# Optimization experiments

Hardware: AMD Instinct MI355X
Metric: run time of the kernel (lower is better)

## Reference

```python
import jax, jax.numpy as jnp
import numpy as np
import math

B, NQ, NKV, D, H, KP = 4, 8192, 8192, 256, 8, 256
HD = D // H


def setup_inputs() -> dict:
    key = jax.random.key(0)
    ks = jax.random.split(key, 8)
    s = 1.0 / math.sqrt(D)
    return {
        "x1": jax.random.normal(ks[0], (B, NQ, D), dtype=jnp.float32),
        "x2": jax.random.normal(ks[1], (NKV, D), dtype=jnp.float32),
        "Wq": jax.random.normal(ks[2], (D, D), dtype=jnp.float32) * s,
        "Wk": jax.random.normal(ks[3], (D, D), dtype=jnp.float32) * s,
        "Wv": jax.random.normal(ks[4], (D, D), dtype=jnp.float32) * s,
        "Wo": jax.random.normal(ks[5], (D, D), dtype=jnp.float32) * s,
        "E": jax.random.normal(ks[6], (NKV, KP), dtype=jnp.float32) * (1.0 / math.sqrt(NKV)),
        "F": jax.random.normal(ks[7], (NKV, KP), dtype=jnp.float32) * (1.0 / math.sqrt(NKV)),
    }


def reference(x1, x2, Wq, Wk, Wv, Wo, E, F):
    # x1: [B, NQ, D] queries; x2: [NKV, D] shared cross-attention context
    q = x1 @ Wq                               # [B, NQ, D]
    k = x2 @ Wk                               # [NKV, D]
    v = x2 @ Wv                               # [NKV, D]
    # Linformer low-rank compression along the KV sequence axis
    k_low = jnp.einsum('nd,nk->kd', k, E)     # [KP, D]
    v_low = jnp.einsum('nd,nk->kd', v, F)     # [KP, D]
    qh = q.reshape(B, NQ, H, HD)
    kh = k_low.reshape(KP, H, HD)
    vh = v_low.reshape(KP, H, HD)
    scale = 1.0 / math.sqrt(HD)
    scores = jnp.einsum('bqhd,khd->bhqk', qh, kh) * scale  # [B, H, NQ, KP]
    attn = jax.nn.softmax(scores, axis=-1)
    out = jnp.einsum('bhqk,khd->bqhd', attn, vh)           # [B, NQ, H, HD]
    out = out.reshape(B, NQ, D)
    return out @ Wo
```

## Files before the change

### kernel.cpp

```cpp
#include <hip/hip_runtime.h>
#include <math.h>
#include <stdint.h>


typedef unsigned short ushort_t;
typedef __attribute__((ext_vector_type(8))) short bf16x8;
typedef __attribute__((ext_vector_type(8))) _Float16 f16x8;
typedef __attribute__((ext_vector_type(4))) float f32x4;

__device__ __forceinline__ f32x4 MFMA(bf16x8 a, bf16x8 b, f32x4 c) {
  return __builtin_amdgcn_mfma_f32_16x16x32_bf16(a, b, c, 0, 0, 0);
}
__device__ __forceinline__ f32x4 MFMA_H(f16x8 a, f16x8 b, f32x4 c) {
  return __builtin_amdgcn_mfma_f32_16x16x32_f16(a, b, c, 0, 0, 0);
}
__device__ __forceinline__ ushort_t f2bf(float x) {
  uint32_t u = __float_as_uint(x);
  u += 0x7fffu + ((u >> 16) & 1u);
  return (ushort_t)(u >> 16);
}
#define GLDS(gsrc, ldst)                                                    \
  __builtin_amdgcn_global_load_lds(                                         \
      (const __attribute__((address_space(1))) uint32_t*)(const void*)(gsrc), \
      (__attribute__((address_space(3))) uint32_t*)(void*)(ldst), 16, 0, 0)

#define STAGE_ROW(u) \
  (((((u) >> 2) ^ ((u) >> 4)) & 1) | (((u) >> 2) & 6) | (((u) >> 5) << 3))
#define STAGE_G(u) \
  ((((u) ^ ((u) >> 2) ^ ((u) >> 4)) & 1) | (((((u) >> 1) ^ ((u) >> 3)) & 1) << 1))

__global__ __launch_bounds__(256) void k_prep_all(
    const float* __restrict__ x2, const float* __restrict__ E,
    const float* __restrict__ F, const float* __restrict__ Wq,
    const float* __restrict__ Wk, const float* __restrict__ Wv,
    const float* __restrict__ Wo, _Float16* __restrict__ xt,
    ushort_t* __restrict__ wqt, ushort_t* __restrict__ wot,
    _Float16* __restrict__ wkt, _Float16* __restrict__ wvt) {
  __shared__ float tile[64][65];
  const int t = threadIdx.x;
  const int z = blockIdx.z;
  if (z < 3) {
    const int n0 = blockIdx.x * 64;
    const int c0 = blockIdx.y * 64;
    const float* __restrict__ src = (z == 0) ? x2 : (z == 1) ? E : F;
    _Float16* __restrict__ dst = xt + (size_t)z * 2097152;
    const int rr = t >> 4, cc = (t & 15) * 4;
#pragma unroll
    for (int i = 0; i < 4; ++i) {
      float4 v = *(const float4*)&src[(size_t)(n0 + rr + 16 * i) * 256 + c0 + cc];
      tile[cc + 0][rr + 16 * i] = v.x;
      tile[cc + 1][rr + 16 * i] = v.y;
      tile[cc + 2][rr + 16 * i] = v.z;
      tile[cc + 3][rr + 16 * i] = v.w;
    }
    __syncthreads();
#pragma unroll
    for (int rnd = 0; rnd < 2; ++rnd) {
      const int u = rnd * 256 + t;
      const int c = u >> 3, r0 = (u & 7) * 8;
      f16x8 h;
#pragma unroll
      for (int j = 0; j < 8; ++j) h[j] = (_Float16)tile[c][r0 + j];
      *(f16x8*)&dst[(size_t)(c0 + c) * 8192 + n0 + r0] = h;
    }
  } else {
    if (blockIdx.x >= 16) return;
    const int m = blockIdx.y;
    const float* __restrict__ src = (m == 0) ? Wq : (m == 1) ? Wo
                                  : (m == 2) ? Wk : Wv;
    const int tr = (blockIdx.x >> 2) * 64;
    const int tc = (blockIdx.x & 3) * 64;
    const int rr = t >> 4, cc = (t & 15) * 4;
#pragma unroll
    for (int i = 0; i < 4; ++i) {
      float4 v = *(const float4*)&src[(size_t)(tr + rr + 16 * i) * 256 + tc + cc];
      tile[cc + 0][rr + 16 * i] = v.x;
      tile[cc + 1][rr + 16 * i] = v.y;
      tile[cc + 2][rr + 16 * i] = v.z;
      tile[cc + 3][rr + 16 * i] = v.w;
    }
    __syncthreads();
#pragma unroll
    for (int rnd = 0; rnd < 2; ++rnd) {
      const int u = rnd * 256 + t;
      const int nl = u >> 3, kl = (u & 7) * 8;
      if (m < 2) {
        const float sc = (m == 0) ? 0.25503488f : 1.0f;
        bf16x8 hv;
#pragma unroll
        for (int j = 0; j < 8; ++j) hv[j] = (short)f2bf(tile[nl][kl + j] * sc);
        ushort_t* dst = (m == 0) ? wqt : wot;
        *(bf16x8*)&dst[(size_t)(tc + nl) * 256 + tr + kl] = hv;
      } else {
        f16x8 hv;
#pragma unroll
        for (int j = 0; j < 8; ++j) hv[j] = (_Float16)tile[nl][kl + j];
        _Float16* dst = (m == 2) ? wkt : wvt;
        *(f16x8*)&dst[(size_t)(tc + nl) * 256 + tr + kl] = hv;
      }
    }
  }
}

__global__ __launch_bounds__(512, 2) void k_mega1(
    const float* __restrict__ x1, const _Float16* __restrict__ xt,
    const ushort_t* __restrict__ wqt, ushort_t* __restrict__ Qf,
    float* __restrict__ part) {
  __shared__ __align__(16) char smem[65536];
  const int t = threadIdx.x;
  const int wv = t >> 6, ln = t & 63;
  const int l15 = ln & 15, g = ln >> 4;

  if (blockIdx.x < 64) {
    const int bid2 = blockIdx.x;
    const int which = bid2 & 1;
    const int chunk = (bid2 >> 1) & 15;
    const int kp0 = (bid2 >> 5) * 128;
    const int n0 = chunk * 512;
    const _Float16* __restrict__ A = xt + (size_t)(1 + which) * 2097152;
    const _Float16* __restrict__ B = xt;
    const int wr = wv >> 2, wc = wv & 3;

    auto stage = [&](int buf, int st) {
#pragma unroll
      for (int r3 = 0; r3 < 3; ++r3) {
        const int u = r3 * 512 + t;
        if (u < 512) {
          const int row = u >> 2, j = u & 3;
          GLDS(A + (size_t)(kp0 + row) * 8192 + n0 + st * 32 +
                   ((j ^ (row & 3)) << 3),
               smem + buf * 24576 + u * 16);
        } else {
          const int uu = u - 512;
          const int row = uu >> 2, j = uu & 3;
          GLDS(B + (size_t)row * 8192 + n0 + st * 32 + ((j ^ (row & 3)) << 3),
               smem + buf * 24576 + 8192 + uu * 16);
        }
      }
    };

    f32x4 acc[4][4];
#pragma unroll
    for (int i = 0; i < 4; ++i)
#pragma unroll
      for (int j = 0; j < 4; ++j) acc[i][j] = {0.f, 0.f, 0.f, 0.f};

    stage(0, 0);
    __syncthreads();
    for (int st = 0; st < 16; ++st) {
      if (st < 15) stage((st + 1) & 1, st + 1);
      const char* la = smem + (st & 1) * 24576;
      const char* lb = la + 8192;
      f16x8 af[4], bf[4];
#pragma unroll
      for (int i = 0; i < 4; ++i) {
        const int ra = wr * 64 + i * 16 + l15;
        af[i] = *(const f16x8*)(la + ra * 64 + ((g ^ (ra & 3)) << 4));
      }
#pragma unroll
      for (int j = 0; j < 4; ++j) {
        const int rb = wc * 64 + j * 16 + l15;
        bf[j] = *(const f16x8*)(lb + rb * 64 + ((g ^ (rb & 3)) << 4));
      }
#pragma unroll
      for (int i = 0; i < 4; ++i)
#pragma unroll
        for (int j = 0; j < 4; ++j) acc[i][j] = MFMA_H(af[i], bf[j], acc[i][j]);
      __syncthreads();
    }
    float* __restrict__ p = part + ((size_t)which * 16 + chunk) * 65536;
#pragma unroll
    for (int i = 0; i < 4; ++i)
#pragma unroll
      for (int j = 0; j < 4; ++j)
#pragma unroll
        for (int r = 0; r < 4; ++r)
          p[(size_t)(kp0 + wr * 64 + i * 16 + g * 4 + r) * 256 + wc * 64 +
            j * 16 + l15] = acc[i][j][r];
  } else {
    const int qb = blockIdx.x - 64;
    const size_t r0 = (size_t)qb * 128;
    auto stageq = [&](int buf, int ks) {
#pragma unroll
      for (int rnd = 0; rnd < 2; ++rnd) {
        const int u = rnd * 512 + t;
        const int n = u >> 2, j = u & 3;
        GLDS(wqt + n * 256 + ks * 32 + ((j ^ (n & 3)) << 3),
             smem + buf * 16384 + u * 16);
      }
    };
    f32x4 qacc[16];
#pragma unroll
    for (int i = 0; i < 16; ++i) qacc[i] = {0.f, 0.f, 0.f, 0.f};
    stageq(0, 0);
    const float* xrow = x1 + (r0 + wv * 16 + l15) * 256;
    float4 a0 = *(const float4*)(xrow + g * 8);
    float4 a1 = *(const float4*)(xrow + g * 8 + 4);
    __syncthreads();

    for (int ks = 0; ks < 8; ++ks) {
      if (ks < 7) stageq((ks + 1) & 1, ks + 1);
      bf16x8 afrag;
      afrag[0] = (short)f2bf(a0.x); afrag[1] = (short)f2bf(a0.y);
      afrag[2] = (short)f2bf(a0.z); afrag[3] = (short)f2bf(a0.w);
      afrag[4] = (short)f2bf(a1.x); afrag[5] = (short)f2bf(a1.y);
      afrag[6] = (short)f2bf(a1.z); afrag[7] = (short)f2bf(a1.w);
      if (ks < 7) {
        a0 = *(const float4*)(xrow + (ks + 1) * 32 + g * 8);
        a1 = *(const float4*)(xrow + (ks + 1) * 32 + g * 8 + 4);
      }
      const char* cw = smem + (ks & 1) * 16384;
#pragma unroll
      for (int tt = 0; tt < 16; ++tt) {
        bf16x8 bfr = *(const bf16x8*)(cw + (tt * 16 + l15) * 64 +
                                      ((g ^ (l15 & 3)) << 4));
        qacc[tt] = MFMA(afrag, bfr, qacc[tt]);
      }
      __syncthreads();
    }
    char* myq = smem + wv * 8192;
#pragma unroll
    for (int tt = 0; tt < 16; ++tt)
#pragma unroll
      for (int r = 0; r < 4; ++r) {
        const int gr = g * 4 + r;
        *(ushort_t*)(myq + gr * 512 +
                     (((tt * 16 + l15) * 2) ^ ((gr & 7) << 4))) =
            f2bf(qacc[tt][r]);
      }
    __builtin_amdgcn_sched_barrier(0);
    const int rt = qb * 8 + wv;
#pragma unroll
    for (int hh = 0; hh < 8; ++hh) {
      bf16x8 qf = *(const bf16x8*)(myq + l15 * 512 +
                                   ((hh * 64 + g * 16) ^ ((l15 & 7) << 4)));
      *(bf16x8*)&Qf[((size_t)(rt * 8 + hh) * 64 + ln) * 8] = qf;
    }
  }
}

__global__ __launch_bounds__(256) void k_reduce_part(
    const float* __restrict__ part, _Float16* __restrict__ ghh) {
  const int oid = blockIdx.x * 256 + threadIdx.x;
  const int which = oid >> 16;
  const int base = oid & 65535;
  const float* __restrict__ p = part + (size_t)which * 16 * 65536 + base;
  float s = 0.f;
#pragma unroll
  for (int c = 0; c < 16; ++c) s += p[c * 65536];
  ghh[oid] = (_Float16)s;
}

__global__ __launch_bounds__(256, 4) void k_lowproj2(
    const _Float16* __restrict__ ghh, const _Float16* __restrict__ wkt,
    const _Float16* __restrict__ wvt, ushort_t* __restrict__ klowA,
    ushort_t* __restrict__ vtb) {
  __shared__ __align__(16) _Float16 wstage[2][4096];
  const int t = threadIdx.x;
  const int wv = t >> 6, ln = t & 63;
  const int l15 = ln & 15, g = ln >> 4;
  const int which = blockIdx.y;
  const int r0 = blockIdx.x * 64;
  const _Float16* __restrict__ A = ghh + (size_t)which * 65536;
  const _Float16* __restrict__ W = which ? wvt : wkt;

  auto stage = [&](int row0, int colu, int buf) {
#pragma unroll
    for (int rnd = 0; rnd < 2; ++rnd) {
      const int u = rnd * 256 + wv * 64 + ln;
      const int row = STAGE_ROW(u);
      const int gg = STAGE_G(u);
      GLDS(W + (size_t)(row0 + row) * 256 + colu + gg * 8,
           &wstage[buf][(rnd * 256 + wv * 64) * 8]);
    }
  };

  f32x4 yacc[16];
#pragma unroll
  for (int i = 0; i < 16; ++i) yacc[i] = {0.f, 0.f, 0.f, 0.f};
  stage(0, 0, 0);
  const _Float16* arow = A + (size_t)(r0 + wv * 16 + l15) * 256;
  __syncthreads();
  for (int ci = 0; ci < 16; ++ci) {
    const int nh = ci & 1, ks = ci >> 1;
    if (ci < 15) stage(((ci + 1) & 1) * 128, ((ci + 1) >> 1) * 32, (ci + 1) & 1);
    f16x8 afrag = *(const f16x8*)(arow + ks * 32 + g * 8);
    const _Float16* cw = wstage[ci & 1];
#pragma unroll
    for (int tt = 0; tt < 8; ++tt) {
      f16x8 bfr = *(const f16x8*)&cw[((tt * 16 + l15) * 32 + g * 8) ^
                                     ((l15 & 7) << 3)];
      yacc[nh * 8 + tt] = MFMA_H(afrag, bfr, yacc[nh * 8 + tt]);
    }
    __syncthreads();
  }
#pragma unroll
  for (int tt = 0; tt < 16; ++tt)
#pragma unroll
    for (int r = 0; r < 4; ++r) {
      const int rowi = r0 + wv * 16 + g * 4 + r;
      const int c = tt * 16 + l15;
      const int hh = c >> 5, d = c & 31;
      const ushort_t val = f2bf(yacc[tt][r]);
      if (which == 0) {
        klowA[(hh << 13) + ((((rowi & 255) << 5) | d) ^ ((rowi & 7) << 3))] = val;
      } else {
        const int kh = (rowi >> 7) & 1, kl = rowi & 127;
        vtb[(((hh * 2 + kh) * 32 + d) << 7) + (kl ^ ((d & 7) << 3))] = val;
      }
    }
}

__global__ __launch_bounds__(512, 4) void k_attn(
    const ushort_t* __restrict__ Qf, const ushort_t* __restrict__ klowA,
    const ushort_t* __restrict__ vtb, ushort_t* __restrict__ O) {
  __shared__ __align__(16) ushort_t kv[16384];
  __shared__ __align__(16) uint32_t p_buf[8][320];
  __shared__ __align__(16) ushort_t o_sl[8][640];
  const int t = threadIdx.x;
  const int wv = t >> 6, ln = t & 63;
  const int l15 = ln & 15, g = ln >> 4;
  const int h = blockIdx.y;
  const size_t r0 = (size_t)blockIdx.x * 512;

  {
    const ushort_t* ksrc = klowA + h * 8192;
    const ushort_t* vsrc = vtb + h * 8192;
#pragma unroll
    for (int rnd = 0; rnd < 2; ++rnd) {
      const int ub = rnd * 512 + wv * 64;
      GLDS(ksrc + (ub + ln) * 8, &kv[ub * 8]);
    }
#pragma unroll
    for (int rnd = 0; rnd < 2; ++rnd) {
      const int ub = rnd * 512 + wv * 64;
      GLDS(vsrc + (ub + ln) * 8, &kv[8192 + ub * 8]);
    }
  }
  __syncthreads();

  for (int st = 0; st < 4; ++st) {
    const int rtb = blockIdx.x * 32 + st * 8 + wv;
    const bf16x8 qfrag = *(const bf16x8*)&Qf[((size_t)(rtb * 8 + h) * 64 + ln) * 8];
    f32x4 s[16];
#pragma unroll
    for (int tt = 0; tt < 16; ++tt) {
      bf16x8 kfr = *(const bf16x8*)&kv[((tt * 16 + l15) * 32 + g * 8) ^
                                       ((l15 & 7) << 3)];
      f32x4 z = {0.f, 0.f, 0.f, 0.f};
      s[tt] = MFMA(kfr, qfrag, z);
    }
    float sum = 0.f;
    uint32_t pw[16][2];
#pragma unroll
    for (int tt = 0; tt < 16; ++tt) {
      float e0 = exp2f(s[tt][0]), e1 = exp2f(s[tt][1]);
      float e2 = exp2f(s[tt][2]), e3 = exp2f(s[tt][3]);
      sum += (e0 + e1) + (e2 + e3);
      pw[tt][0] = (uint32_t)f2bf(e0) | ((uint32_t)f2bf(e1) << 16);
      pw[tt][1] = (uint32_t)f2bf(e2) | ((uint32_t)f2bf(e3) << 16);
    }
    sum += __shfl_xor(sum, 16);
    sum += __shfl_xor(sum, 32);
    const float rinv = 1.0f / sum;
    float rv[4];
#pragma unroll
    for (int r = 0; r < 4; ++r) rv[r] = __shfl(rinv, g * 4 + r);

    f32x4 oacc[2];
    oacc[0] = {0.f, 0.f, 0.f, 0.f};
    oacc[1] = {0.f, 0.f, 0.f, 0.f};
    uint32_t* pbw = &p_buf[wv][l15 * 20];
#pragma unroll
    for (int kh = 0; kh < 2; ++kh) {
      const char* cv = (const char*)&kv[8192 + kh * 4096];
#pragma unroll
      for (int ksl = 0; ksl < 4; ++ksl) {
        const int ks = kh * 4 + ksl;
        pbw[2 * g + 0] = pw[2 * ks][0];
        pbw[2 * g + 1] = pw[2 * ks][1];
        pbw[8 + 2 * g + 0] = pw[2 * ks + 1][0];
        pbw[8 + 2 * g + 1] = pw[2 * ks + 1][1];
        __builtin_amdgcn_sched_barrier(0);
        bf16x8 pfr = *(const bf16x8*)&p_buf[wv][l15 * 20 + 4 * g];
#pragma unroll
        for (int nt = 0; nt < 2; ++nt) {
          bf16x8 vfr = *(const bf16x8*)(cv + (nt * 16 + l15) * 256 +
                                        ((ksl * 64 + g * 16) ^ ((l15 & 7) << 4)));
          oacc[nt] = MFMA(pfr, vfr, oacc[nt]);
        }
        __builtin_amdgcn_sched_barrier(0);
      }
    }
#pragma unroll
    for (int nt = 0; nt < 2; ++nt)
#pragma unroll
      for (int r = 0; r < 4; ++r)
        o_sl[wv][(g * 4 + r) * 40 + nt * 16 + l15] = f2bf(oacc[nt][r] * rv[r]);
    __builtin_amdgcn_sched_barrier(0);
    {
      const int qr = ln >> 2, d0 = (ln & 3) * 8;
      bf16x8 ov = *(const bf16x8*)&o_sl[wv][qr * 40 + d0];
      *(bf16x8*)&O[(r0 + st * 128 + wv * 16 + qr) * 256 + h * 32 + d0] = ov;
    }
    __builtin_amdgcn_sched_barrier(0);
  }
}

__global__ __launch_bounds__(512, 2) void k_ogemm(
    const ushort_t* __restrict__ O, const ushort_t* __restrict__ wot,
    float* __restrict__ out) {
  __shared__ __align__(16) char smem[32768];
  const int t = threadIdx.x;
  const int wv = t >> 6, ln = t & 63;
  const int l15 = ln & 15, g = ln >> 4;
  const size_t r0 = (size_t)blockIdx.x * 128;

  auto stageo = [&](int buf, int ks) {
#pragma unroll
    for (int rnd = 0; rnd < 2; ++rnd) {
      const int u = rnd * 512 + t;
      const int n = u >> 2, j = u & 3;
      GLDS(wot + n * 256 + ks * 32 + ((j ^ (n & 3)) << 3),
           smem + buf * 16384 + u * 16);
    }
  };

  f32x4 yacc[16];
#pragma unroll
  for (int i = 0; i < 16; ++i) yacc[i] = {0.f, 0.f, 0.f, 0.f};
  stageo(0, 0);
  const ushort_t* arow = O + (r0 + wv * 16 + l15) * 256;
  bf16x8 afrag = *(const bf16x8*)(arow + g * 8);
  __syncthreads();

  for (int ks = 0; ks < 8; ++ks) {
    if (ks < 7) stageo((ks + 1) & 1, ks + 1);
    bf16x8 cA = afrag;
    if (ks < 7) afrag = *(const bf16x8*)(arow + (ks + 1) * 32 + g * 8);
    const char* cw = smem + (ks & 1) * 16384;
#pragma unroll
    for (int tt = 0; tt < 16; ++tt) {
      bf16x8 bfr = *(const bf16x8*)(cw + (tt * 16 + l15) * 64 +
                                    ((g ^ (l15 & 3)) << 4));
      yacc[tt] = MFMA(cA, bfr, yacc[tt]);
    }
    __syncthreads();
  }
#pragma unroll
  for (int tt = 0; tt < 16; ++tt)
#pragma unroll
    for (int r = 0; r < 4; ++r)
      out[(r0 + wv * 16 + g * 4 + r) * 256 + tt * 16 + l15] = yacc[tt][r];
}

extern "C" void kernel_launch(void* const* d_in, const int* in_sizes, int n_in,
                              void* d_out, int out_size, void* d_ws, size_t ws_size,
                              hipStream_t stream) {
  const float* x1 = (const float*)d_in[0];
  const float* x2 = (const float*)d_in[1];
  const float* Wq = (const float*)d_in[2];
  const float* Wk = (const float*)d_in[3];
  const float* Wv = (const float*)d_in[4];
  const float* Wo = (const float*)d_in[5];
  const float* E  = (const float*)d_in[6];
  const float* F  = (const float*)d_in[7];
  float* out = (float*)d_out;
  float* ws = (float*)d_ws;
  _Float16* ghh = (_Float16*)ws;
  ushort_t* wqt = (ushort_t*)(ws + 65536);
  ushort_t* wot = (ushort_t*)(ws + 98304);
  _Float16* wkt = (_Float16*)(ws + 131072);
  _Float16* wvt = (_Float16*)(ws + 163840);
  ushort_t* klowA = (ushort_t*)(ws + 196608);
  ushort_t* vtb = (ushort_t*)(ws + 229376);
  float* part = ws + 262144;
  ushort_t* Qf = (ushort_t*)(ws + 2359296);
  _Float16* xt = (_Float16*)(ws + 6553600);
  ushort_t* O = (ushort_t*)(ws + 6553600);

  k_prep_all<<<dim3(128, 4, 4), 256, 0, stream>>>(x2, E, F, Wq, Wk, Wv, Wo, xt,
                                                  wqt, wot, wkt, wvt);
  k_mega1<<<320, 512, 0, stream>>>(x1, xt, wqt, Qf, part);
  k_reduce_part<<<512, 256, 0, stream>>>(part, ghh);
  k_lowproj2<<<dim3(4, 2), 256, 0, stream>>>(ghh, wkt, wvt, klowA, vtb);
  k_attn<<<dim3(64, 8), 512, 0, stream>>>(Qf, klowA, vtb, O);
  k_ogemm<<<256, 512, 0, stream>>>(O, wot, out);
}
```

Before: 94.43 us.

## Fuse attention and output projection into one kernel with per-wave heads

Merges the attention kernel and the Wo output GEMM into a single kernel. Each block handles 64 rows with one wave per head, keeps the attention output in LDS instead of writing O to global memory, then runs the output projection from LDS. K/V fragments are now read straight from global memory instead of being staged in shared memory. This removes a launch and the round trip of the intermediate O buffer, but gives up LDS reuse of K/V and lowers occupancy.

```diff
diff --git a/kernel.cpp b/kernel.cpp
--- a/kernel.cpp
+++ b/kernel.cpp
@@ -311,44 +311,49 @@
     }
 }
 
-__global__ __launch_bounds__(512, 4) void k_attn(
+__global__ __launch_bounds__(512, 2) void k_attn_out(
     const ushort_t* __restrict__ Qf, const ushort_t* __restrict__ klowA,
-    const ushort_t* __restrict__ vtb, ushort_t* __restrict__ O) {
-  __shared__ __align__(16) ushort_t kv[16384];
+    const ushort_t* __restrict__ vtb, const ushort_t* __restrict__ wot,
+    float* __restrict__ out) {
+  __shared__ __align__(16) char o_lds[32768];
+  __shared__ __align__(16) char wstage[32768];
   __shared__ __align__(16) uint32_t p_buf[8][320];
-  __shared__ __align__(16) ushort_t o_sl[8][640];
   const int t = threadIdx.x;
   const int wv = t >> 6, ln = t & 63;
   const int l15 = ln & 15, g = ln >> 4;
-  const int h = blockIdx.y;
-  const size_t r0 = (size_t)blockIdx.x * 512;
-
-  {
-    const ushort_t* ksrc = klowA + h * 8192;
-    const ushort_t* vsrc = vtb + h * 8192;
+  const size_t r0 = (size_t)blockIdx.x * 64;
+  const int h = wv;
+
+  auto stageo = [&](int buf, int ks) {
 #pragma unroll
     for (int rnd = 0; rnd < 2; ++rnd) {
-      const int ub = rnd * 512 + wv * 64;
-      GLDS(ksrc + (ub + ln) * 8, &kv[ub * 8]);
-    }
-#pragma unroll
-    for (int rnd = 0; rnd < 2; ++rnd) {
-      const int ub = rnd * 512 + wv * 64;
-      GLDS(vsrc + (ub + ln) * 8, &kv[8192 + ub * 8]);
-    }
-  }
-  __syncthreads();
-
+      const int u = rnd * 512 + t;
+      const int n = u >> 2, j = u & 3;
+      GLDS(wot + n * 256 + ks * 32 + ((j ^ (n & 3)) << 3),
+           wstage + buf * 16384 + u * 16);
+    }
+  };
+
+  stageo(0, 0);
+
+  const ushort_t* kh_ = klowA + h * 8192;
+  const ushort_t* vh_ = vtb + h * 8192;
+  bf16x8 qfr[4];
+#pragma unroll
   for (int st = 0; st < 4; ++st) {
-    const int rtb = blockIdx.x * 32 + st * 8 + wv;
-    const bf16x8 qfrag = *(const bf16x8*)&Qf[((size_t)(rtb * 8 + h) * 64 + ln) * 8];
+    const int rt = blockIdx.x * 4 + st;
+    qfr[st] = *(const bf16x8*)&Qf[((size_t)(rt * 8 + h) * 64 + ln) * 8];
+  }
+
+#pragma unroll
+  for (int st = 0; st < 4; ++st) {
     f32x4 s[16];
 #pragma unroll
     for (int tt = 0; tt < 16; ++tt) {
-      bf16x8 kfr = *(const bf16x8*)&kv[((tt * 16 + l15) * 32 + g * 8) ^
-                                       ((l15 & 7) << 3)];
+      bf16x8 kfr = *(const bf16x8*)&kh_[(((tt * 16 + l15) * 32 + g * 8)) ^
+                                        ((l15 & 7) << 3)];
       f32x4 z = {0.f, 0.f, 0.f, 0.f};
-      s[tt] = MFMA(kfr, qfrag, z);
+      s[tt] = MFMA(kfr, qfr[st], z);
     }
     float sum = 0.f;
     uint32_t pw[16][2];
@@ -372,11 +377,11 @@
     oacc[1] = {0.f, 0.f, 0.f, 0.f};
     uint32_t* pbw = &p_buf[wv][l15 * 20];
 #pragma unroll
-    for (int kh = 0; kh < 2; ++kh) {
-      const char* cv = (const char*)&kv[8192 + kh * 4096];
+    for (int kh2 = 0; kh2 < 2; ++kh2) {
+      const char* cv = (const char*)(vh_ + kh2 * 4096);
 #pragma unroll
       for (int ksl = 0; ksl < 4; ++ksl) {
-        const int ks = kh * 4 + ksl;
+        const int ks = kh2 * 4 + ksl;
         pbw[2 * g + 0] = pw[2 * ks][0];
         pbw[2 * g + 1] = pw[2 * ks][1];
         pbw[8 + 2 * g + 0] = pw[2 * ks + 1][0];
@@ -395,63 +400,40 @@
 #pragma unroll
     for (int nt = 0; nt < 2; ++nt)
 #pragma unroll
-      for (int r = 0; r < 4; ++r)
-        o_sl[wv][(g * 4 + r) * 40 + nt * 16 + l15] = f2bf(oacc[nt][r] * rv[r]);
-    __builtin_amdgcn_sched_barrier(0);
-    {
-      const int qr = ln >> 2, d0 = (ln & 3) * 8;
-      bf16x8 ov = *(const bf16x8*)&o_sl[wv][qr * 40 + d0];
-      *(bf16x8*)&O[(r0 + st * 128 + wv * 16 + qr) * 256 + h * 32 + d0] = ov;
-    }
-    __builtin_amdgcn_sched_barrier(0);
-  }
-}
-
-__global__ __launch_bounds__(512, 2) void k_ogemm(
-    const ushort_t* __restrict__ O, const ushort_t* __restrict__ wot,
-    float* __restrict__ out) {
-  __shared__ __align__(16) char smem[32768];
-  const int t = threadIdx.x;
-  const int wv = t >> 6, ln = t & 63;
-  const int l15 = ln & 15, g = ln >> 4;
-  const size_t r0 = (size_t)blockIdx.x * 128;
-
-  auto stageo = [&](int buf, int ks) {
-#pragma unroll
-    for (int rnd = 0; rnd < 2; ++rnd) {
-      const int u = rnd * 512 + t;
-      const int n = u >> 2, j = u & 3;
-      GLDS(wot + n * 256 + ks * 32 + ((j ^ (n & 3)) << 3),
-           smem + buf * 16384 + u * 16);
-    }
-  };
-
-  f32x4 yacc[16];
-#pragma unroll
-  for (int i = 0; i < 16; ++i) yacc[i] = {0.f, 0.f, 0.f, 0.f};
-  stageo(0, 0);
-  const ushort_t* arow = O + (r0 + wv * 16 + l15) * 256;
-  bf16x8 afrag = *(const bf16x8*)(arow + g * 8);
+      for (int r = 0; r < 4; ++r) {
+        const int row = st * 16 + g * 4 + r;
+        const int cb = (h * 32 + nt * 16 + l15) * 2;
+        *(ushort_t*)(o_lds + row * 512 + (cb ^ ((row & 7) << 4))) =
+            f2bf(oacc[nt][r] * rv[r]);
+      }
+  }
   __syncthreads();
+
+  const int rg = wv >> 1, ch = wv & 1;
+  const int arow = rg * 16 + l15;
+  f32x4 yacc[8];
+#pragma unroll
+  for (int i = 0; i < 8; ++i) yacc[i] = {0.f, 0.f, 0.f, 0.f};
 
   for (int ks = 0; ks < 8; ++ks) {
     if (ks < 7) stageo((ks + 1) & 1, ks + 1);
-    bf16x8 cA = afrag;
-    if (ks < 7) afrag = *(const bf16x8*)(arow + (ks + 1) * 32 + g * 8);
-    const char* cw = smem + (ks & 1) * 16384;
-#pragma unroll
-    for (int tt = 0; tt < 16; ++tt) {
-      bf16x8 bfr = *(const bf16x8*)(cw + (tt * 16 + l15) * 64 +
-                                    ((g ^ (l15 & 3)) << 4));
-      yacc[tt] = MFMA(cA, bfr, yacc[tt]);
-    }
-    __syncthreads();
-  }
-#pragma unroll
-  for (int tt = 0; tt < 16; ++tt)
+    bf16x8 afrag = *(const bf16x8*)(o_lds + arow * 512 +
+                                    ((ks * 64 + g * 16) ^ ((arow & 7) << 4)));
+    const char* cw = wstage + (ks & 1) * 16384;
+#pragma unroll
+    for (int tt = 0; tt < 8; ++tt) {
+      const int n = ch * 128 + tt * 16 + l15;
+      bf16x8 bfr = *(const bf16x8*)(cw + n * 64 + ((g ^ (n & 3)) << 4));
+      yacc[tt] = MFMA(afrag, bfr, yacc[tt]);
+    }
+    __syncthreads();
+  }
+#pragma unroll
+  for (int tt = 0; tt < 8; ++tt)
 #pragma unroll
     for (int r = 0; r < 4; ++r)
-      out[(r0 + wv * 16 + g * 4 + r) * 256 + tt * 16 + l15] = yacc[tt][r];
+      out[(r0 + rg * 16 + g * 4 + r) * 256 + ch * 128 + tt * 16 + l15] =
+          yacc[tt][r];
 }
 
 extern "C" void kernel_launch(void* const* d_in, const int* in_sizes, int n_in,
@@ -477,13 +459,11 @@
   float* part = ws + 262144;
   ushort_t* Qf = (ushort_t*)(ws + 2359296);
   _Float16* xt = (_Float16*)(ws + 6553600);
-  ushort_t* O = (ushort_t*)(ws + 6553600);
 
   k_prep_all<<<dim3(128, 4, 4), 256, 0, stream>>>(x2, E, F, Wq, Wk, Wv, Wo, xt,
                                                   wqt, wot, wkt, wvt);
   k_mega1<<<320, 512, 0, stream>>>(x1, xt, wqt, Qf, part);
   k_reduce_part<<<512, 256, 0, stream>>>(part, ghh);
   k_lowproj2<<<dim3(4, 2), 256, 0, stream>>>(ghh, wkt, wvt, klowA, vtb);
-  k_attn<<<dim3(64, 8), 512, 0, stream>>>(Qf, klowA, vtb, O);
-  k_ogemm<<<256, 512, 0, stream>>>(O, wot, out);
-}
+  k_attn_out<<<512, 512, 0, stream>>>(Qf, klowA, vtb, wot, out);
+}
```

Result: slower. 96.87 us (+2.6%).
